# Kernel tuning notes

Hardware: AMD Instinct MI355X
Metric: run time of the kernel (lower is better)

Reference implementation:

```python
import jax, jax.numpy as jnp
import numpy as np

V, E, H = 32000, 256, 512

def gru_cell(x, h, W_ih, W_hh, b_ih, b_hh):
    # PyTorch GRU cell: gates ordered (r, z, n)
    gi = x @ W_ih.T + b_ih
    gh = h @ W_hh.T + b_hh
    i_r, i_z, i_n = jnp.split(gi, 3, axis=-1)
    h_r, h_z, h_n = jnp.split(gh, 3, axis=-1)
    r = jax.nn.sigmoid(i_r + h_r)
    z = jax.nn.sigmoid(i_z + h_z)
    n = jnp.tanh(i_n + r * h_n)
    return (1.0 - z) * n + z * h


def setup_inputs() -> dict:
    key = jax.random.key(0)
    ks = jax.random.split(key, 16)
    B, Tx, Ty = 32, 512, 128
    s = lambda k, sh: jax.random.normal(k, sh, jnp.float32) * 0.05
    return {
        "x": jax.random.randint(ks[0], (B, Tx), 0, V),
        "y": jax.random.randint(ks[1], (B, Ty), 0, V),
        "embedding": s(ks[2], (V, E)),
        "enc_W_ih": s(ks[3], (3 * H, E)),
        "enc_W_hh": s(ks[4], (3 * H, H)),
        "enc_b_ih": s(ks[5], (3 * H,)),
        "enc_b_hh": s(ks[6], (3 * H,)),
        "dec_W_ih": s(ks[7], (3 * H, E + H)),
        "dec_W_hh": s(ks[8], (3 * H, H)),
        "dec_b_ih": s(ks[9], (3 * H,)),
        "dec_b_hh": s(ks[10], (3 * H,)),
        "h_init": s(ks[11], (1, H)),
        "fc_W": s(ks[12], (V, H)),
        "fc_b": s(ks[13], (V,)),
    }


def reference(x, y, embedding, enc_W_ih, enc_W_hh, enc_b_ih, enc_b_hh,
              dec_W_ih, dec_W_hh, dec_b_ih, dec_b_hh, h_init, fc_W, fc_b):
    B = x.shape[0]
    # ---- encode ----
    ex = embedding[x]  # [B, Tx, E]
    def enc_step(h, xt):
        h2 = gru_cell(xt, h, enc_W_ih, enc_W_hh, enc_b_ih, enc_b_hh)
        return h2, h2
    h0 = jnp.zeros((B, H), ex.dtype)
    _, eh = jax.lax.scan(enc_step, h0, jnp.swapaxes(ex, 0, 1))
    eh = jnp.swapaxes(eh, 0, 1)  # [B, Tx, H]

    # ---- decode with per-step dot-product attention ----
    inputs = embedding[y[:, :-1]]  # [B, Ty-1, E]
    ox0 = jnp.broadcast_to(h_init, (B, H)).astype(ex.dtype)
    hx0 = jnp.zeros((B, H), ex.dtype)
    def dec_step(carry, it):
        ox, hx = carry
        scores = jnp.einsum('bth,bh->bt', eh, ox)       # dot-product attention
        a = jax.nn.softmax(scores, axis=1)              # softmax over time
        sx = jnp.einsum('bth,bt->bh', eh, a)            # context summary
        ix = jnp.concatenate([it, sx], axis=-1)         # [B, E+H]
        hx2 = gru_cell(ix, hx, dec_W_ih, dec_W_hh, dec_b_ih, dec_b_hh)
        return (hx2, hx2), hx2 + sx                     # ox = dec output = hx (1 layer)
    _, outs = jax.lax.scan(dec_step, (ox0, hx0), jnp.swapaxes(inputs, 0, 1))
    out = jnp.swapaxes(outs, 0, 1)  # [B, Ty-1, H]
    return out @ fc_W.T + fc_b      # [B, Ty-1, V]
```

## Files before the change

kernel.cpp:

```cpp
#include <hip/hip_runtime.h>
#include <hip/hip_bf16.h>


#define B_  32
#define TX_ 512
#define TY_ 127
#define E_  256
#define H_  512
#define G3_ 1536
#define V_  32000
#define NA_ 128
#define NW_ 32
#define NF_ 80

typedef unsigned short u16;
typedef short short8 __attribute__((ext_vector_type(8)));
typedef float f32x4 __attribute__((ext_vector_type(4)));
typedef float f32x2 __attribute__((ext_vector_type(2)));
typedef unsigned int u32x4 __attribute__((ext_vector_type(4)));

__device__ __forceinline__ float bfu(u16 h){ union{unsigned u; float f;} x; x.u=((unsigned)h)<<16; return x.f; }
__device__ __forceinline__ u16 f2bf(float f){ union{float f; unsigned u;} v; v.f=f; unsigned r=v.u+0x7fffu+((v.u>>16)&1u); return (u16)(r>>16); }
__device__ __forceinline__ float sigm(float x){ return 1.f/(1.f+__expf(-x)); }
__device__ __forceinline__ float tanh_f(float x){ return 1.f - 2.f/(__expf(2.f*x)+1.f); }

__device__ __forceinline__ u32x4 ld16_c(const void* p){
  u32x4 r;
  asm volatile("global_load_dwordx4 %0, %1, off sc0 sc1\n\ts_waitcnt vmcnt(0)"
               : "=v"(r) : "v"(p) : "memory");
  return r;
}
__device__ __forceinline__ void st_u16_c(void* p, unsigned v){
  asm volatile("global_store_short %0, %1, off sc0 sc1" :: "v"(p), "v"(v) : "memory");
}
__device__ __forceinline__ void st8_c(void* p, float a, float b){
  f32x2 v; v.x=a; v.y=b;
  asm volatile("global_store_dwordx2 %0, %1, off sc0 sc1" :: "v"(p), "v"(v) : "memory");
}
__device__ __forceinline__ void st4f_c(void* p, float v){
  asm volatile("global_store_dword %0, %1, off sc0 sc1" :: "v"(p), "v"(v) : "memory");
}

__device__ __forceinline__ void spin_rel(int* p, int tgt){
  int n = 0;
  while (__hip_atomic_load(p, __ATOMIC_RELAXED, __HIP_MEMORY_SCOPE_AGENT) < tgt){
    __builtin_amdgcn_s_sleep(1);
    if (++n > (1<<22)) break;
  }
}
__device__ __forceinline__ void spin_rel_slow(int* p, int tgt){
  int n = 0;
  while (__hip_atomic_load(p, __ATOMIC_RELAXED, __HIP_MEMORY_SCOPE_AGENT) < tgt){
    __builtin_amdgcn_s_sleep(16);
    if (++n > (1<<20)) break;
  }
}

__device__ __forceinline__ void stage4_c(u16 (*stgl)[520], const u16* src, int tid){
  const u16* b0 = src + (size_t)(tid>>6)*H_ + (tid&63)*8;
  const u16* b1 = b0 + (size_t)8*H_;
  const u16* b2 = b0 + (size_t)16*H_;
  const u16* b3 = b0 + (size_t)24*H_;
  u32x4 q0,q1,q2,q3;
  asm volatile(
    "global_load_dwordx4 %0, %4, off sc0 sc1\n\t"
    "global_load_dwordx4 %1, %5, off sc0 sc1\n\t"
    "global_load_dwordx4 %2, %6, off sc0 sc1\n\t"
    "global_load_dwordx4 %3, %7, off sc0 sc1\n\t"
    "s_waitcnt vmcnt(0)"
    : "=&v"(q0),"=&v"(q1),"=&v"(q2),"=&v"(q3)
    : "v"(b0),"v"(b1),"v"(b2),"v"(b3) : "memory");
  int r = tid>>6, c = (tid&63)*8;
  *(u32x4*)&stgl[r][c]    = q0;
  *(u32x4*)&stgl[r+8][c]  = q1;
  *(u32x4*)&stgl[r+16][c] = q2;
  *(u32x4*)&stgl[r+24][c] = q3;
}

__global__ void cvt_rows(const float* __restrict__ src, int sld, int soff,
                         u16* __restrict__ dst, int cols){
  int r = blockIdx.x;
  const float* s = src + (size_t)r*sld + soff;
  u16* d = dst + (size_t)r*cols;
  for (int c = threadIdx.x; c < cols; c += blockDim.x) d[c] = f2bf(s[c]);
}

__global__ void gather_embed(const float* __restrict__ emb, const int* __restrict__ idx,
                             u16* __restrict__ dst, int rows_per_b, int ld){
  int m = blockIdx.x;
  int bb = m / rows_per_b, tt = m - bb*rows_per_b;
  int id = idx[bb*ld + tt];
  dst[(size_t)m*E_ + threadIdx.x] = f2bf(emb[(size_t)id*E_ + threadIdx.x]);
}

__global__ __launch_bounds__(256) void gemm_bf16(
    const u16* __restrict__ A, int lda, const u16* __restrict__ Bm, int ldb,
    void* __restrict__ Cout, int ldc, const float* __restrict__ bias,
    int M, int K, int out_bf16)
{
  int wave = threadIdx.x >> 6, lane = threadIdx.x & 63;
  int m0 = blockIdx.x*128 + (wave>>1)*64;
  int n0 = blockIdx.y*128 + (wave&1)*64;
  int lr = lane & 15, lk = (lane>>4)*8;
  f32x4 acc[4][4];
  #pragma unroll
  for (int i=0;i<4;++i)
    #pragma unroll
    for (int j=0;j<4;++j) acc[i][j] = (f32x4){0.f,0.f,0.f,0.f};
  for (int k0=0; k0<K; k0+=32){
    short8 af[4], bfv[4];
    #pragma unroll
    for (int i=0;i<4;++i){
      int row = m0 + i*16 + lr; if (row > M-1) row = M-1;
      af[i] = *(const short8*)(A + (size_t)row*lda + k0 + lk);
    }
    #pragma unroll
    for (int j=0;j<4;++j){
      int col = n0 + j*16 + lr;
      bfv[j] = *(const short8*)(Bm + (size_t)col*ldb + k0 + lk);
    }
    #pragma unroll
    for (int i=0;i<4;++i)
      #pragma unroll
      for (int j=0;j<4;++j)
        acc[i][j] = __builtin_amdgcn_mfma_f32_16x16x32_bf16(af[i], bfv[j], acc[i][j], 0,0,0);
  }
  int rbase = (lane>>4)*4;
  #pragma unroll
  for (int i=0;i<4;++i)
    #pragma unroll
    for (int r=0;r<4;++r){
      int row = m0 + i*16 + rbase + r;
      if (row < M){
        #pragma unroll
        for (int j=0;j<4;++j){
          int col = n0 + j*16 + lr;
          float v = acc[i][j][r] + bias[col];
          if (out_bf16) ((u16*)Cout)[(size_t)row*ldc + col] = f2bf(v);
          else          ((float*)Cout)[(size_t)row*ldc + col] = v;
        }
      }
    }
}

__global__ __launch_bounds__(512,2) void enc_v3(
    const u16* __restrict__ Gx, const u16* __restrict__ Whh_bf,
    const float* __restrict__ bhh, u16* __restrict__ eh,
    u16* __restrict__ hgd, int* flags)
{
  __shared__ __align__(16) u16 stgl[32][520];
  __shared__ __align__(16) float gH[32][52];
  int tid = threadIdx.x, g = blockIdx.x;
  int wave = tid>>6, lane = tid&63;
  int pb = tid>>4, pu = tid&15, u = g*16 + pu;

  short8 fH[16];
  int mt = wave/3, nt = wave%3;
  if (wave < 6){
    int row = nt*H_ + g*16 + (lane&15);
    int kb = (lane>>4)*8;
    #pragma unroll
    for (int ks=0;ks<16;++ks)
      fH[ks] = *(const short8*)(Whh_bf + (size_t)row*H_ + ks*32 + kb);
  }
  float bhR = bhh[u], bhZ = bhh[u+H_], bhN = bhh[u+2*H_];
  float hloc = 0.f;
  size_t gx0 = (size_t)pb*TX_*G3_;
  float iR = bfu(Gx[gx0+u]), iZ = bfu(Gx[gx0+H_+u]), iN = bfu(Gx[gx0+2*H_+u]);

  for (int t=0;t<TX_;++t){
    if (t > 0){
      if (tid < 32) spin_rel(&flags[tid], t);
      __syncthreads();
      asm volatile("" ::: "memory");
    }
    stage4_c(stgl, hgd + (size_t)(t&1)*B_*H_, tid);
    __syncthreads();
    if (wave < 6){
      f32x4 acc = (f32x4){0.f,0.f,0.f,0.f};
      int ar = mt*16 + (lane&15), ak = (lane>>4)*8;
      #pragma unroll
      for (int ks=0;ks<16;++ks)
        acc = __builtin_amdgcn_mfma_f32_16x16x32_bf16(*(const short8*)&stgl[ar][ks*32+ak], fH[ks], acc, 0,0,0);
      int dr = mt*16 + ((lane>>4)<<2), dc = nt*16 + (lane&15);
      #pragma unroll
      for (int r=0;r<4;++r) gH[dr+r][dc] = acc[r];
    }
    __syncthreads();
    float r = sigm(iR + gH[pb][pu]    + bhR);
    float z = sigm(iZ + gH[pb][16+pu] + bhZ);
    float n = tanh_f(iN + r*(gH[pb][32+pu] + bhN));
    hloc = (1.f-z)*n + z*hloc;
    u16 hb = f2bf(hloc);
    st_u16_c(&hgd[(size_t)((t+1)&1)*B_*H_ + (size_t)pb*H_ + u], (unsigned)hb);
    __syncthreads();
    if (tid == 0)
      __hip_atomic_store(&flags[blockIdx.x], t+1, __ATOMIC_RELAXED, __HIP_MEMORY_SCOPE_AGENT);
    eh[((size_t)pb*TX_ + t)*H_ + u] = hb;
    if (t+1 < TX_){
      size_t g2 = ((size_t)pb*TX_ + (t+1))*G3_;
      iR = bfu(Gx[g2+u]); iZ = bfu(Gx[g2+H_+u]); iN = bfu(Gx[g2+2*H_+u]);
    }
  }
}

__global__ __launch_bounds__(512,2) void dec_v5(
    const u16* __restrict__ eh, const u16* __restrict__ Gy,
    const u16* __restrict__ WihS_bf, const u16* __restrict__ Whh_bf,
    const float* __restrict__ dbhh, const float* __restrict__ hinit,
    const u16* __restrict__ Wfc_bf, const float* __restrict__ fcB,
    u16* __restrict__ sxb, u16* __restrict__ hdd2,
    float* __restrict__ part, float* __restrict__ statsg,
    u16* __restrict__ XfcT, float* __restrict__ out,
    int* Pf, int* Xf, int* Hf, int* ticket)
{
  struct AS {
    u16   ehq[128][512];
    u16   oxb[512];
    float sc[128];
    float pt[8][512];
    float red[16];
  };
  struct WS { u16 stgl[32][520]; float gS[32][52]; float gH[32][52]; };
  struct FS { u16 Ab[128][520]; int tkS; };
  __shared__ __align__(16) char smem_[sizeof(AS)];
  int tid = threadIdx.x;
  int wave = tid>>6, lane = tid&63;

  if (blockIdx.x < NA_){
    AS& S = *(AS*)smem_;
    int b = blockIdx.x >> 2, q = blockIdx.x & 3;
    {
      const u16* ehg = eh + ((size_t)b*TX_ + q*128)*H_;
      int row = tid>>2, c0 = (tid&3)*128;
      #pragma unroll
      for (int j=0;j<16;++j){
        int u0 = c0 + j*8;
        uint4 v = *(const uint4*)(ehg + (size_t)row*H_ + u0);
        *(uint4*)&S.ehq[row][u0 ^ ((row&7)<<3)] = v;
      }
    }
    __syncthreads();
    bool bl = (lane&15) == 0;
    for (int t=0;t<TY_;++t){
      if (t > 0){
        if (tid < NW_) spin_rel(&Hf[tid], t);
        __syncthreads();
        asm volatile("" ::: "memory");
        if (tid < 64){
          u32x4 qv = ld16_c(hdd2 + (size_t)(t&1)*B_*H_ + (size_t)b*H_ + tid*8);
          *(u32x4*)&S.oxb[tid*8] = qv;
        }
      } else {
        S.oxb[tid] = f2bf(hinit[tid]);
      }
      __syncthreads();
      {
        f32x4 acS = (f32x4){0.f,0.f,0.f,0.f};
        int arow = wave*16 + (lane&15);
        int swz = (arow&7)<<3;
        #pragma unroll
        for (int kt=0;kt<16;++kt){
          short8 bf = (short8){0,0,0,0,0,0,0,0};
          if (bl) bf = *(const short8*)&S.oxb[kt*32 + (lane>>4)*8];
          short8 af_ = *(const short8*)&S.ehq[arow][(kt*32 + (lane>>4)*8) ^ swz];
          acS = __builtin_amdgcn_mfma_f32_16x16x32_bf16(af_, bf, acS, 0,0,0);
        }
        if (bl){
          #pragma unroll
          for (int r=0;r<4;++r) S.sc[wave*16 + (lane>>4)*4 + r] = acS[r];
        }
      }
      __syncthreads();
      float mq, lq;
      {
        float v = (tid<128) ? S.sc[tid] : -3e38f;
        #pragma unroll
        for (int o=32;o>0;o>>=1) v = fmaxf(v, __shfl_xor(v, o));
        if (lane==0) S.red[wave] = v;
        __syncthreads();
        mq = fmaxf(S.red[0], S.red[1]);
        float e = 0.f;
        if (tid<128){ e = __expf(S.sc[tid] - mq); S.sc[tid] = e; }
        float s2 = e;
        #pragma unroll
        for (int o=32;o>0;o>>=1) s2 += __shfl_xor(s2, o);
        if (lane==0) S.red[8+wave] = s2;
        __syncthreads();
        lq = S.red[8] + S.red[9];
      }
      int u0 = lane*8, tseg = wave;
      f32x4 aLo = (f32x4){0.f,0.f,0.f,0.f}, aHi = (f32x4){0.f,0.f,0.f,0.f};
      #pragma unroll
      for (int j=0;j<16;++j){
        int tp = tseg*16 + j;
        short8 ev = *(const short8*)&S.ehq[tp][u0 ^ ((tp&7)<<3)];
        float av = S.sc[tp];
        aLo[0] = fmaf(bfu((u16)ev[0]), av, aLo[0]);
        aLo[1] = fmaf(bfu((u16)ev[1]), av, aLo[1]);
        aLo[2] = fmaf(bfu((u16)ev[2]), av, aLo[2]);
        aLo[3] = fmaf(bfu((u16)ev[3]), av, aLo[3]);
        aHi[0] = fmaf(bfu((u16)ev[4]), av, aHi[0]);
        aHi[1] = fmaf(bfu((u16)ev[5]), av, aHi[1]);
        aHi[2] = fmaf(bfu((u16)ev[6]), av, aHi[2]);
        aHi[3] = fmaf(bfu((u16)ev[7]), av, aHi[3]);
      }
      *(f32x4*)&S.pt[tseg][u0]   = aLo;
      *(f32x4*)&S.pt[tseg][u0+4] = aHi;
      __syncthreads();
      float sv = 0.f;
      #pragma unroll
      for (int gsg=0; gsg<8; ++gsg) sv += S.pt[gsg][tid];
      if (q != 0){
        st4f_c(&part[(size_t)(b*4+q)*512 + tid], sv);
        if (tid==0) st8_c(&statsg[(size_t)(b*4+q)*2], mq, lq);
        __syncthreads();
        if (tid==0) __hip_atomic_store(&Pf[b*4+q], t+1, __ATOMIC_RELAXED, __HIP_MEMORY_SCOPE_AGENT);
      } else {
        if (tid < 3) spin_rel(&Pf[b*4+1+tid], t+1);
        __syncthreads();
        asm volatile("" ::: "memory");
        float p1,p2,p3; f32x2 s1,s2,s3;
        {
          const float* pp1 = &part[(size_t)(b*4+1)*512 + tid];
          const float* pp2 = &part[(size_t)(b*4+2)*512 + tid];
          const float* pp3 = &part[(size_t)(b*4+3)*512 + tid];
          const float* ps1 = &statsg[(size_t)(b*4+1)*2];
          const float* ps2 = &statsg[(size_t)(b*4+2)*2];
          const float* ps3 = &statsg[(size_t)(b*4+3)*2];
          asm volatile(
            "global_load_dword %0, %6, off sc0 sc1\n\t"
            "global_load_dword %1, %7, off sc0 sc1\n\t"
            "global_load_dword %2, %8, off sc0 sc1\n\t"
            "global_load_dwordx2 %3, %9, off sc0 sc1\n\t"
            "global_load_dwordx2 %4, %10, off sc0 sc1\n\t"
            "global_load_dwordx2 %5, %11, off sc0 sc1\n\t"
            "s_waitcnt vmcnt(0)"
            : "=&v"(p1),"=&v"(p2),"=&v"(p3),"=&v"(s1),"=&v"(s2),"=&v"(s3)
            : "v"(pp1),"v"(pp2),"v"(pp3),"v"(ps1),"v"(ps2),"v"(ps3) : "memory");
        }
        float gmax = fmaxf(fmaxf(mq,s1.x), fmaxf(s2.x,s3.x));
        float e0=__expf(mq-gmax), e1=__expf(s1.x-gmax), e2=__expf(s2.x-gmax), e3=__expf(s3.x-gmax);
        float inv = 1.f/(lq*e0 + s1.y*e1 + s2.y*e2 + s3.y*e3);
        float sx = (sv*e0 + p1*e1 + p2*e2 + p3*e3) * inv;
        st_u16_c(&sxb[(size_t)b*H_ + tid], (unsigned)f2bf(sx));
        __syncthreads();
        if (tid==0) __hip_atomic_store(&Xf[b], t+1, __ATOMIC_RELAXED, __HIP_MEMORY_SCOPE_AGENT);
      }
    }
  } else if (blockIdx.x < NA_ + NW_){
    WS& S = *(WS*)smem_;
    int g = blockIdx.x - NA_;
    int pb = tid>>4, pu = tid&15, u = g*16 + pu;
    short8 fS[16], fH[16];
    int mt = wave/3, nt = wave%3;
    if (wave < 6){
      int row = nt*H_ + g*16 + (lane&15);
      int kb = (lane>>4)*8;
      #pragma unroll
      for (int ks=0;ks<16;++ks){
        fS[ks] = *(const short8*)(WihS_bf + (size_t)row*H_ + ks*32 + kb);
        fH[ks] = *(const short8*)(Whh_bf  + (size_t)row*H_ + ks*32 + kb);
      }
    }
    float bhR = dbhh[u], bhZ = dbhh[u+H_], bhN = dbhh[u+2*H_];
    float hloc = 0.f;

    for (int t=0;t<TY_;++t){
      size_t gyb = ((size_t)pb*TY_ + t)*G3_;
      float iR = bfu(Gy[gyb+u]), iZ = bfu(Gy[gyb+H_+u]), iN = bfu(Gy[gyb+2*H_+u]);
      if (tid < NW_) spin_rel(&Hf[tid], t);
      __syncthreads();
      asm volatile("" ::: "memory");
      stage4_c(S.stgl, hdd2 + (size_t)(t&1)*B_*H_, tid);
      __syncthreads();
      int ar = mt*16 + (lane&15), ak = (lane>>4)*8;
      if (wave < 6){
        f32x4 acc = (f32x4){0.f,0.f,0.f,0.f};
        #pragma unroll
        for (int ks=0;ks<16;++ks)
          acc = __builtin_amdgcn_mfma_f32_16x16x32_bf16(*(const short8*)&S.stgl[ar][ks*32+ak], fH[ks], acc, 0,0,0);
        int dr = mt*16 + ((lane>>4)<<2), dc = nt*16 + (lane&15);
        #pragma unroll
        for (int r=0;r<4;++r) S.gH[dr+r][dc] = acc[r];
      }
      if (tid < 32) spin_rel(&Xf[tid], t+1);
      __syncthreads();
      asm volatile("" ::: "memory");
      stage4_c(S.stgl, sxb, tid);
      __syncthreads();
      float sxv = bfu(S.stgl[pb][u]);
      if (wave < 6){
        f32x4 acc = (f32x4){0.f,0.f,0.f,0.f};
        #pragma unroll
        for (int ks=0;ks<16;++ks)
          acc = __builtin_amdgcn_mfma_f32_16x16x32_bf16(*(const short8*)&S.stgl[ar][ks*32+ak], fS[ks], acc, 0,0,0);
        int dr = mt*16 + ((lane>>4)<<2), dc = nt*16 + (lane&15);
        #pragma unroll
        for (int r=0;r<4;++r) S.gS[dr+r][dc] = acc[r];
      }
      __syncthreads();
      {
        float r = sigm(iR + S.gS[pb][pu]    + S.gH[pb][pu]    + bhR);
        float z = sigm(iZ + S.gS[pb][16+pu] + S.gH[pb][16+pu] + bhZ);
        float n = tanh_f(iN + S.gS[pb][32+pu] + r*(S.gH[pb][32+pu] + bhN));
        hloc = (1.f-z)*n + z*hloc;
        st_u16_c(&hdd2[(size_t)((t+1)&1)*B_*H_ + (size_t)pb*H_ + u], (unsigned)f2bf(hloc));
        st_u16_c(&XfcT[((size_t)t*B_ + pb)*H_ + u], (unsigned)f2bf(hloc + sxv));
      }
      __syncthreads();
      if (tid==0) __hip_atomic_store(&Hf[g], t+1, __ATOMIC_RELAXED, __HIP_MEMORY_SCOPE_AGENT);
    }
  } else {
    FS& S = *(FS*)smem_;
    int lr = lane & 15, lk = (lane>>4)*8;
    int m0 = (wave>>2)*64, n0w = (wave&3)*64;
    while (true){
      if (tid == 0)
        S.tkS = __hip_atomic_fetch_add(ticket, 1, __ATOMIC_RELAXED, __HIP_MEMORY_SCOPE_AGENT);
      __syncthreads();
      int tk = S.tkS;
      __syncthreads();
      if (tk >= 32*32) break;
      int tb = tk >> 5, c = tk & 31;
      int nbase = c*4;
      int nbend = (nbase+4 < 125) ? nbase+4 : 125;
      int te = 4*tb + 4; if (te > TY_) te = TY_;
      if (tid < NW_) spin_rel_slow(&Hf[tid], te);
      __syncthreads();
      asm volatile("" ::: "memory");
      {
        const u16* src = XfcT + (size_t)tb*128*H_;
        #pragma unroll
        for (int it2=0; it2<16; ++it2){
          int el = (it2*512 + tid)*8;
          int rr = el >> 9, cc = el & 511;
          u32x4 v = ld16_c(src + (size_t)rr*H_ + cc);
          *(u32x4*)&S.Ab[rr][cc] = v;
        }
      }
      __syncthreads();
      for (int nb = nbase; nb < nbend; ++nb){
        int ncol0 = nb*256 + n0w;
        f32x4 acc[4][4];
        #pragma unroll
        for (int i=0;i<4;++i)
          #pragma unroll
          for (int j=0;j<4;++j) acc[i][j] = (f32x4){0.f,0.f,0.f,0.f};
        for (int k0=0; k0<H_; k0+=32){
          short8 af[4], bfv[4];
          #pragma unroll
          for (int i=0;i<4;++i)
            af[i] = *(const short8*)&S.Ab[m0 + i*16 + lr][k0 + lk];
          #pragma unroll
          for (int j=0;j<4;++j)
            bfv[j] = *(const short8*)(Wfc_bf + (size_t)(ncol0 + j*16 + lr)*H_ + k0 + lk);
          #pragma unroll
          for (int i=0;i<4;++i)
            #pragma unroll
            for (int j=0;j<4;++j)
              acc[i][j] = __builtin_amdgcn_mfma_f32_16x16x32_bf16(af[i], bfv[j], acc[i][j], 0,0,0);
        }
        int rbase = (lane>>4)*4;
        #pragma unroll
        for (int i=0;i<4;++i)
          #pragma unroll
          for (int r=0;r<4;++r){
            int arow = m0 + i*16 + rbase + r;
            int t2 = tb*4 + (arow>>5), b2 = arow&31;
            if (t2 < TY_){
              #pragma unroll
              for (int j=0;j<4;++j){
                int col = ncol0 + j*16 + lr;
                out[((size_t)b2*TY_ + t2)*V_ + col] = acc[i][j][r] + fcB[col];
              }
            }
          }
        __syncthreads();
      }
    }
  }
}

extern "C" void kernel_launch(void* const* d_in, const int* in_sizes, int n_in,
                              void* d_out, int out_size, void* d_ws, size_t ws_size,
                              hipStream_t stream) {
  const int*   x     = (const int*)d_in[0];
  const int*   y     = (const int*)d_in[1];
  const float* emb   = (const float*)d_in[2];
  const float* eWih  = (const float*)d_in[3];
  const float* eWhh  = (const float*)d_in[4];
  const float* eBih  = (const float*)d_in[5];
  const float* eBhh  = (const float*)d_in[6];
  const float* dWih  = (const float*)d_in[7];
  const float* dWhh  = (const float*)d_in[8];
  const float* dBih  = (const float*)d_in[9];
  const float* dBhh  = (const float*)d_in[10];
  const float* hinit = (const float*)d_in[11];
  const float* fcW   = (const float*)d_in[12];
  const float* fcB   = (const float*)d_in[13];
  float* out = (float*)d_out;
  (void)in_sizes; (void)n_in; (void)out_size; (void)ws_size;

  char* p = (char*)d_ws;
  auto take = [&](size_t bytes)->char*{ char* r = p; p += (bytes + 255) & ~(size_t)255; return r; };
  u16* Wfc_bf   = (u16*)take((size_t)V_*H_*2);
  u16* ex_bf    = (u16*)take((size_t)B_*TX_*E_*2);
  u16* eWih_bf  = (u16*)take((size_t)G3_*E_*2);
  u16* Gx_bf    = (u16*)take((size_t)B_*TX_*G3_*2);
  u16* eh_bf    = (u16*)take((size_t)B_*TX_*H_*2);
  u16* embY_bf  = (u16*)take((size_t)4096*E_*2);
  u16* dWihE_bf = (u16*)take((size_t)G3_*E_*2);
  u16* Gy_bf    = (u16*)take((size_t)4096*G3_*2);
  u16* XfcT_bf  = (u16*)take((size_t)4096*H_*2);
  u16* eWhh_bf  = (u16*)take((size_t)G3_*H_*2);
  u16* dWhh_bf  = (u16*)take((size_t)G3_*H_*2);
  u16* dWihS_bf = (u16*)take((size_t)G3_*H_*2);
  u16* hgd      = (u16*)take((size_t)2*B_*H_*2);
  u16* hdd2     = (u16*)take((size_t)2*B_*H_*2);
  u16* sxb      = (u16*)take((size_t)B_*H_*2);
  float* part   = (float*)take((size_t)NA_*H_*4);
  float* statsg = (float*)take((size_t)NA_*2*4);
  int* flagsE   = (int*)take(256);
  int* ctrl     = (int*)take(4096);
  int* Pf = ctrl, *Xf = ctrl+128, *Hf = ctrl+160, *ticket = ctrl+200;

  hipMemsetAsync(flagsE, 0, 256, stream);
  hipMemsetAsync(ctrl, 0, 4096, stream);
  hipMemsetAsync(hgd, 0, (size_t)2*B_*H_*2, stream);
  hipMemsetAsync(hdd2, 0, (size_t)2*B_*H_*2, stream);

  cvt_rows<<<dim3(V_),  dim3(256), 0, stream>>>(fcW,  H_, 0, Wfc_bf,   H_);
  cvt_rows<<<dim3(G3_), dim3(256), 0, stream>>>(eWih, E_, 0, eWih_bf,  E_);
  cvt_rows<<<dim3(G3_), dim3(256), 0, stream>>>(dWih, E_+H_, 0, dWihE_bf, E_);
  cvt_rows<<<dim3(G3_), dim3(256), 0, stream>>>(eWhh, H_, 0, eWhh_bf,  H_);
  cvt_rows<<<dim3(G3_), dim3(256), 0, stream>>>(dWhh, H_, 0, dWhh_bf,  H_);
  cvt_rows<<<dim3(G3_), dim3(256), 0, stream>>>(dWih, E_+H_, E_, dWihS_bf, H_);

  gather_embed<<<dim3(B_*TX_), dim3(E_), 0, stream>>>(emb, x, ex_bf, TX_, TX_);
  gather_embed<<<dim3(B_*TY_), dim3(E_), 0, stream>>>(emb, y, embY_bf, TY_, 128);

  gemm_bf16<<<dim3(B_*TX_/128, G3_/128), dim3(256), 0, stream>>>(
      ex_bf, E_, eWih_bf, E_, Gx_bf, G3_, eBih, B_*TX_, E_, 1);
  gemm_bf16<<<dim3(32, G3_/128), dim3(256), 0, stream>>>(
      embY_bf, E_, dWihE_bf, E_, Gy_bf, G3_, dBih, B_*TY_, E_, 1);

  enc_v3<<<dim3(32), dim3(512), 0, stream>>>(Gx_bf, eWhh_bf, eBhh, eh_bf, hgd, flagsE);

  dec_v5<<<dim3(NA_+NW_+NF_), dim3(512), 0, stream>>>(
      eh_bf, Gy_bf, dWihS_bf, dWhh_bf, dBhh, hinit, Wfc_bf, fcB,
      sxb, hdd2, part, statsg, XfcT_bf, out, Pf, Xf, Hf, ticket);
}
```

Baseline: 2.684 ms.

## Merge attention partials directly in GRU blocks, removing a sync hop per decode step

Attention blocks now write bf16 partial context sums and softmax stats straight to global memory. The GRU worker blocks wait on all 128 partial flags and do the cross-quarter softmax merge themselves, so the extra q==0 combine stage and its Xf flag round-trip on the sequential decode path are gone. The six weight-conversion launches and the two embedding-gather launches are each fused into one kernel to cut launch overhead. In exchange, every GRU block now spins on 128 flags and redundantly reads all partials each step, and storing partials in bf16 reduces precision.

```diff
diff --git a/kernel.cpp b/kernel.cpp
--- a/kernel.cpp
+++ b/kernel.cpp
@@ -20,6 +20,8 @@
 typedef unsigned int u32x4 __attribute__((ext_vector_type(4)));
 
 __device__ __forceinline__ float bfu(u16 h){ union{unsigned u; float f;} x; x.u=((unsigned)h)<<16; return x.f; }
+__device__ __forceinline__ float bflo(unsigned p){ union{unsigned u; float f;} x; x.u=p<<16; return x.f; }
+__device__ __forceinline__ float bfhi(unsigned p){ union{unsigned u; float f;} x; x.u=p&0xffff0000u; return x.f; }
 __device__ __forceinline__ u16 f2bf(float f){ union{float f; unsigned u;} v; v.f=f; unsigned r=v.u+0x7fffu+((v.u>>16)&1u); return (u16)(r>>16); }
 __device__ __forceinline__ float sigm(float x){ return 1.f/(1.f+__expf(-x)); }
 __device__ __forceinline__ float tanh_f(float x){ return 1.f - 2.f/(__expf(2.f*x)+1.f); }
@@ -30,15 +32,29 @@
                : "=v"(r) : "v"(p) : "memory");
   return r;
 }
+__device__ __forceinline__ f32x2 ld8_c(const void* p){
+  f32x2 r;
+  asm volatile("global_load_dwordx2 %0, %1, off sc0 sc1\n\ts_waitcnt vmcnt(0)"
+               : "=v"(r) : "v"(p) : "memory");
+  return r;
+}
+__device__ __forceinline__ void ld4x16_c(const u16* a, const u16* b, const u16* c, const u16* d,
+                                         u32x4& q0, u32x4& q1, u32x4& q2, u32x4& q3){
+  asm volatile(
+    "global_load_dwordx4 %0, %4, off sc0 sc1\n\t"
+    "global_load_dwordx4 %1, %5, off sc0 sc1\n\t"
+    "global_load_dwordx4 %2, %6, off sc0 sc1\n\t"
+    "global_load_dwordx4 %3, %7, off sc0 sc1\n\t"
+    "s_waitcnt vmcnt(0)"
+    : "=&v"(q0),"=&v"(q1),"=&v"(q2),"=&v"(q3)
+    : "v"(a),"v"(b),"v"(c),"v"(d) : "memory");
+}
 __device__ __forceinline__ void st_u16_c(void* p, unsigned v){
   asm volatile("global_store_short %0, %1, off sc0 sc1" :: "v"(p), "v"(v) : "memory");
 }
 __device__ __forceinline__ void st8_c(void* p, float a, float b){
   f32x2 v; v.x=a; v.y=b;
   asm volatile("global_store_dwordx2 %0, %1, off sc0 sc1" :: "v"(p), "v"(v) : "memory");
-}
-__device__ __forceinline__ void st4f_c(void* p, float v){
-  asm volatile("global_store_dword %0, %1, off sc0 sc1" :: "v"(p), "v"(v) : "memory");
 }
 
 __device__ __forceinline__ void spin_rel(int* p, int tgt){
@@ -77,20 +93,37 @@
   *(u32x4*)&stgl[r+24][c] = q3;
 }
 
-__global__ void cvt_rows(const float* __restrict__ src, int sld, int soff,
-                         u16* __restrict__ dst, int cols){
+__global__ void cvt_all(const float* __restrict__ fcW, const float* __restrict__ eWih,
+                        const float* __restrict__ dWih, const float* __restrict__ eWhh,
+                        const float* __restrict__ dWhh,
+                        u16* __restrict__ Wfc, u16* __restrict__ eWihB, u16* __restrict__ dWihE,
+                        u16* __restrict__ eWhhB, u16* __restrict__ dWhhB, u16* __restrict__ dWihS){
   int r = blockIdx.x;
-  const float* s = src + (size_t)r*sld + soff;
-  u16* d = dst + (size_t)r*cols;
-  for (int c = threadIdx.x; c < cols; c += blockDim.x) d[c] = f2bf(s[c]);
-}
-
-__global__ void gather_embed(const float* __restrict__ emb, const int* __restrict__ idx,
-                             u16* __restrict__ dst, int rows_per_b, int ld){
+  const float* s; u16* d; int cols, sld, soff;
+  if      (r < V_)        {            s=fcW;  d=Wfc;   cols=H_; sld=H_;    soff=0;  }
+  else if (r < V_+G3_)    { r-=V_;     s=eWih; d=eWihB; cols=E_; sld=E_;    soff=0;  }
+  else if (r < V_+2*G3_)  { r-=V_+G3_; s=dWih; d=dWihE; cols=E_; sld=E_+H_; soff=0;  }
+  else if (r < V_+3*G3_)  { r-=V_+2*G3_; s=eWhh; d=eWhhB; cols=H_; sld=H_;  soff=0;  }
+  else if (r < V_+4*G3_)  { r-=V_+3*G3_; s=dWhh; d=dWhhB; cols=H_; sld=H_;  soff=0;  }
+  else                    { r-=V_+4*G3_; s=dWih; d=dWihS; cols=H_; sld=E_+H_; soff=E_; }
+  const float* sp = s + (size_t)r*sld + soff;
+  u16* dp = d + (size_t)r*cols;
+  for (int c = threadIdx.x; c < cols; c += blockDim.x) dp[c] = f2bf(sp[c]);
+}
+
+__global__ void gather_all(const float* __restrict__ emb, const int* __restrict__ x,
+                           const int* __restrict__ y, u16* __restrict__ ex,
+                           u16* __restrict__ embY){
   int m = blockIdx.x;
-  int bb = m / rows_per_b, tt = m - bb*rows_per_b;
-  int id = idx[bb*ld + tt];
-  dst[(size_t)m*E_ + threadIdx.x] = f2bf(emb[(size_t)id*E_ + threadIdx.x]);
+  if (m < B_*TX_){
+    int id = x[m];
+    ex[(size_t)m*E_ + threadIdx.x] = f2bf(emb[(size_t)id*E_ + threadIdx.x]);
+  } else {
+    m -= B_*TX_;
+    int bb = m / TY_, tt = m - bb*TY_;
+    int id = y[bb*128 + tt];
+    embY[(size_t)m*E_ + threadIdx.x] = f2bf(emb[(size_t)id*E_ + threadIdx.x]);
+  }
 }
 
 __global__ __launch_bounds__(256) void gemm_bf16(
@@ -204,15 +237,14 @@
   }
 }
 
-__global__ __launch_bounds__(512,2) void dec_v5(
+__global__ __launch_bounds__(512,2) void dec_v6(
     const u16* __restrict__ eh, const u16* __restrict__ Gy,
     const u16* __restrict__ WihS_bf, const u16* __restrict__ Whh_bf,
     const float* __restrict__ dbhh, const float* __restrict__ hinit,
     const u16* __restrict__ Wfc_bf, const float* __restrict__ fcB,
-    u16* __restrict__ sxb, u16* __restrict__ hdd2,
-    float* __restrict__ part, float* __restrict__ statsg,
-    u16* __restrict__ XfcT, float* __restrict__ out,
-    int* Pf, int* Xf, int* Hf, int* ticket)
+    u16* __restrict__ part_bf, float* __restrict__ statsg,
+    u16* __restrict__ hdd2, u16* __restrict__ XfcT, float* __restrict__ out,
+    int* Pf, int* Hf, int* ticket)
 {
   struct AS {
     u16   ehq[128][512];
@@ -221,7 +253,12 @@
     float pt[8][512];
     float red[16];
   };
-  struct WS { u16 stgl[32][520]; float gS[32][52]; float gH[32][52]; };
+  struct WS {
+    u16 stgl[32][520];
+    float gS[32][52]; float gH[32][52];
+    float stf[256];
+    float scl[32][4];
+  };
   struct FS { u16 Ab[128][520]; int tkS; };
   __shared__ __align__(16) char smem_[sizeof(AS)];
   int tid = threadIdx.x;
@@ -311,42 +348,10 @@
       float sv = 0.f;
       #pragma unroll
       for (int gsg=0; gsg<8; ++gsg) sv += S.pt[gsg][tid];
-      if (q != 0){
-        st4f_c(&part[(size_t)(b*4+q)*512 + tid], sv);
-        if (tid==0) st8_c(&statsg[(size_t)(b*4+q)*2], mq, lq);
-        __syncthreads();
-        if (tid==0) __hip_atomic_store(&Pf[b*4+q], t+1, __ATOMIC_RELAXED, __HIP_MEMORY_SCOPE_AGENT);
-      } else {
-        if (tid < 3) spin_rel(&Pf[b*4+1+tid], t+1);
-        __syncthreads();
-        asm volatile("" ::: "memory");
-        float p1,p2,p3; f32x2 s1,s2,s3;
-        {
-          const float* pp1 = &part[(size_t)(b*4+1)*512 + tid];
-          const float* pp2 = &part[(size_t)(b*4+2)*512 + tid];
-          const float* pp3 = &part[(size_t)(b*4+3)*512 + tid];
-          const float* ps1 = &statsg[(size_t)(b*4+1)*2];
-          const float* ps2 = &statsg[(size_t)(b*4+2)*2];
-          const float* ps3 = &statsg[(size_t)(b*4+3)*2];
-          asm volatile(
-            "global_load_dword %0, %6, off sc0 sc1\n\t"
-            "global_load_dword %1, %7, off sc0 sc1\n\t"
-            "global_load_dword %2, %8, off sc0 sc1\n\t"
-            "global_load_dwordx2 %3, %9, off sc0 sc1\n\t"
-            "global_load_dwordx2 %4, %10, off sc0 sc1\n\t"
-            "global_load_dwordx2 %5, %11, off sc0 sc1\n\t"
-            "s_waitcnt vmcnt(0)"
-            : "=&v"(p1),"=&v"(p2),"=&v"(p3),"=&v"(s1),"=&v"(s2),"=&v"(s3)
-            : "v"(pp1),"v"(pp2),"v"(pp3),"v"(ps1),"v"(ps2),"v"(ps3) : "memory");
-        }
-        float gmax = fmaxf(fmaxf(mq,s1.x), fmaxf(s2.x,s3.x));
-        float e0=__expf(mq-gmax), e1=__expf(s1.x-gmax), e2=__expf(s2.x-gmax), e3=__expf(s3.x-gmax);
-        float inv = 1.f/(lq*e0 + s1.y*e1 + s2.y*e2 + s3.y*e3);
-        float sx = (sv*e0 + p1*e1 + p2*e2 + p3*e3) * inv;
-        st_u16_c(&sxb[(size_t)b*H_ + tid], (unsigned)f2bf(sx));
-        __syncthreads();
-        if (tid==0) __hip_atomic_store(&Xf[b], t+1, __ATOMIC_RELAXED, __HIP_MEMORY_SCOPE_AGENT);
-      }
+      st_u16_c(&part_bf[(size_t)(b*4+q)*512 + tid], (unsigned)f2bf(sv));
+      if (tid==0) st8_c(&statsg[(size_t)(b*4+q)*2], mq, lq);
+      __syncthreads();
+      if (tid==0) __hip_atomic_store(&Pf[b*4+q], t+1, __ATOMIC_RELAXED, __HIP_MEMORY_SCOPE_AGENT);
     }
   } else if (blockIdx.x < NA_ + NW_){
     WS& S = *(WS*)smem_;
@@ -384,10 +389,47 @@
         #pragma unroll
         for (int r=0;r<4;++r) S.gH[dr+r][dc] = acc[r];
       }
-      if (tid < 32) spin_rel(&Xf[tid], t+1);
+      if (tid < 128) spin_rel(&Pf[tid], t+1);
       __syncthreads();
       asm volatile("" ::: "memory");
-      stage4_c(S.stgl, sxb, tid);
+      if (tid < 128){
+        f32x2 r2 = ld8_c(&statsg[(size_t)tid*2]);
+        S.stf[tid*2] = r2.x; S.stf[tid*2+1] = r2.y;
+      }
+      __syncthreads();
+      if (tid < 32){
+        float m0=S.stf[(tid*4+0)*2], l0=S.stf[(tid*4+0)*2+1];
+        float m1=S.stf[(tid*4+1)*2], l1=S.stf[(tid*4+1)*2+1];
+        float m2=S.stf[(tid*4+2)*2], l2=S.stf[(tid*4+2)*2+1];
+        float m3=S.stf[(tid*4+3)*2], l3=S.stf[(tid*4+3)*2+1];
+        float gm = fmaxf(fmaxf(m0,m1), fmaxf(m2,m3));
+        float e0=__expf(m0-gm), e1=__expf(m1-gm), e2=__expf(m2-gm), e3=__expf(m3-gm);
+        float inv = 1.f/(l0*e0 + l1*e1 + l2*e2 + l3*e3);
+        S.scl[tid][0]=e0*inv; S.scl[tid][1]=e1*inv; S.scl[tid][2]=e2*inv; S.scl[tid][3]=e3*inv;
+      }
+      __syncthreads();
+      {
+        int r = tid>>4, cg0 = (tid&15)*32;
+        float s0=S.scl[r][0], s1=S.scl[r][1], s2=S.scl[r][2], s3=S.scl[r][3];
+        #pragma unroll
+        for (int cg=0; cg<4; ++cg){
+          int c0 = cg0 + cg*8;
+          const u16* p0 = part_bf + ((size_t)(r*4+0))*512 + c0;
+          const u16* p1 = part_bf + ((size_t)(r*4+1))*512 + c0;
+          const u16* p2 = part_bf + ((size_t)(r*4+2))*512 + c0;
+          const u16* p3 = part_bf + ((size_t)(r*4+3))*512 + c0;
+          u32x4 q0,q1,q2,q3;
+          ld4x16_c(p0,p1,p2,p3,q0,q1,q2,q3);
+          u32x4 pk;
+          #pragma unroll
+          for (int w=0;w<4;++w){
+            float vlo = bflo(q0[w])*s0 + bflo(q1[w])*s1 + bflo(q2[w])*s2 + bflo(q3[w])*s3;
+            float vhi = bfhi(q0[w])*s0 + bfhi(q1[w])*s1 + bfhi(q2[w])*s2 + bfhi(q3[w])*s3;
+            pk[w] = (unsigned)f2bf(vlo) | ((unsigned)f2bf(vhi) << 16);
+          }
+          *(u32x4*)&S.stgl[r][c0] = pk;
+        }
+      }
       __syncthreads();
       float sxv = bfu(S.stgl[pb][u]);
       if (wave < 6){
@@ -518,27 +560,22 @@
   u16* dWihS_bf = (u16*)take((size_t)G3_*H_*2);
   u16* hgd      = (u16*)take((size_t)2*B_*H_*2);
   u16* hdd2     = (u16*)take((size_t)2*B_*H_*2);
-  u16* sxb      = (u16*)take((size_t)B_*H_*2);
-  float* part   = (float*)take((size_t)NA_*H_*4);
+  u16* part_bf  = (u16*)take((size_t)NA_*H_*2);
   float* statsg = (float*)take((size_t)NA_*2*4);
   int* flagsE   = (int*)take(256);
   int* ctrl     = (int*)take(4096);
-  int* Pf = ctrl, *Xf = ctrl+128, *Hf = ctrl+160, *ticket = ctrl+200;
+  int* Pf = ctrl, *Hf = ctrl+160, *ticket = ctrl+200;
 
   hipMemsetAsync(flagsE, 0, 256, stream);
   hipMemsetAsync(ctrl, 0, 4096, stream);
   hipMemsetAsync(hgd, 0, (size_t)2*B_*H_*2, stream);
   hipMemsetAsync(hdd2, 0, (size_t)2*B_*H_*2, stream);
 
-  cvt_rows<<<dim3(V_),  dim3(256), 0, stream>>>(fcW,  H_, 0, Wfc_bf,   H_);
-  cvt_rows<<<dim3(G3_), dim3(256), 0, stream>>>(eWih, E_, 0, eWih_bf,  E_);
-  cvt_rows<<<dim3(G3_), dim3(256), 0, stream>>>(dWih, E_+H_, 0, dWihE_bf, E_);
-  cvt_rows<<<dim3(G3_), dim3(256), 0, stream>>>(eWhh, H_, 0, eWhh_bf,  H_);
-  cvt_rows<<<dim3(G3_), dim3(256), 0, stream>>>(dWhh, H_, 0, dWhh_bf,  H_);
-  cvt_rows<<<dim3(G3_), dim3(256), 0, stream>>>(dWih, E_+H_, E_, dWihS_bf, H_);
-
-  gather_embed<<<dim3(B_*TX_), dim3(E_), 0, stream>>>(emb, x, ex_bf, TX_, TX_);
-  gather_embed<<<dim3(B_*TY_), dim3(E_), 0, stream>>>(emb, y, embY_bf, TY_, 128);
+  cvt_all<<<dim3(V_ + 5*G3_), dim3(256), 0, stream>>>(
+      fcW, eWih, dWih, eWhh, dWhh,
+      Wfc_bf, eWih_bf, dWihE_bf, eWhh_bf, dWhh_bf, dWihS_bf);
+
+  gather_all<<<dim3(B_*TX_ + B_*TY_), dim3(256), 0, stream>>>(emb, x, y, ex_bf, embY_bf);
 
   gemm_bf16<<<dim3(B_*TX_/128, G3_/128), dim3(256), 0, stream>>>(
       ex_bf, E_, eWih_bf, E_, Gx_bf, G3_, eBih, B_*TX_, E_, 1);
@@ -547,7 +584,7 @@
 
   enc_v3<<<dim3(32), dim3(512), 0, stream>>>(Gx_bf, eWhh_bf, eBhh, eh_bf, hgd, flagsE);
 
-  dec_v5<<<dim3(NA_+NW_+NF_), dim3(512), 0, stream>>>(
+  dec_v6<<<dim3(NA_+NW_+NF_), dim3(512), 0, stream>>>(
       eh_bf, Gy_bf, dWihS_bf, dWhh_bf, dBhh, hinit, Wfc_bf, fcB,
-      sxb, hdd2, part, statsg, XfcT_bf, out, Pf, Xf, Hf, ticket);
-}
+      part_bf, statsg, hdd2, XfcT_bf, out, Pf, Hf, ticket);
+}
```

After: 2.933 ms. 9.2% more time.
